# Optimization experiments

Measured on AMD Instinct MI355X. Metric: run time of the kernel, lower is better.

## Reference

```python
import jax, jax.numpy as jnp
import numpy as np

DIM = 512
HEADS = 8
DIM_HEAD = 64
INNER = HEADS * DIM_HEAD  # 512
NARROW_K = 9
WIDE_K = 9
WIDE_DIL = 5


def setup_inputs() -> dict:
    key = jax.random.key(0)
    ks = jax.random.split(key, 12)
    b, n = 4, 2048
    s = lambda fan_in: 1.0 / np.sqrt(fan_in)
    inp = {
        'tokens': jax.random.normal(ks[0], (b, n, DIM), jnp.float32),
        'mask': jax.random.randint(ks[1], (b, n), 0, 2) > 0,
        'w_qkv': jax.random.normal(ks[2], (DIM, INNER * 3), jnp.float32) * s(DIM),
        'w_out': jax.random.normal(ks[3], (INNER, DIM), jnp.float32) * s(INNER),
        'b_out': jnp.zeros((DIM,), jnp.float32),
        'w_narrow': jax.random.normal(ks[4], (DIM, DIM, NARROW_K), jnp.float32) * s(DIM * NARROW_K),
        'b_narrow': jnp.zeros((DIM,), jnp.float32),
        'w_wide': jax.random.normal(ks[5], (DIM, DIM, WIDE_K), jnp.float32) * s(DIM * WIDE_K),
        'b_wide': jnp.zeros((DIM,), jnp.float32),
        'ln1_g': jnp.ones((DIM,), jnp.float32),
        'ln1_b': jnp.zeros((DIM,), jnp.float32),
        'ff_w': jax.random.normal(ks[6], (DIM, DIM), jnp.float32) * s(DIM),
        'ff_b': jnp.zeros((DIM,), jnp.float32),
        'ln2_g': jnp.ones((DIM,), jnp.float32),
        'ln2_b': jnp.zeros((DIM,), jnp.float32),
    }
    return inp


def layer_norm(x, g, b, eps=1e-5):
    m = jnp.mean(x, axis=-1, keepdims=True)
    v = jnp.mean(jnp.square(x - m), axis=-1, keepdims=True)
    return (x - m) / jnp.sqrt(v + eps) * g + b


def rope_encoding(seq_len, dim_head, dtype):
    inv_freq = 1.0 / (10000.0 ** (jnp.arange(0, dim_head, 2, dtype=jnp.float32) / dim_head))
    pos = jnp.arange(seq_len, dtype=jnp.float32)
    sinu = jnp.einsum('i,j->ij', pos, inv_freq)  # [n, d/2]
    return jnp.concatenate([jnp.sin(sinu), jnp.cos(sinu)], axis=-1).astype(dtype)  # [n, d]


def attn(tokens, mask, w_qkv, w_out, b_out):
    b, n, _ = tokens.shape
    qkv = tokens @ w_qkv  # [b, n, 3*inner]
    q, k, v = jnp.split(qkv, 3, axis=-1)
    reshp = lambda t: t.reshape(b, n, HEADS, DIM_HEAD).transpose(0, 2, 1, 3)  # b h n d
    q, k, v = reshp(q), reshp(k), reshp(v)
    rope = rope_encoding(n, DIM_HEAD, tokens.dtype)  # [n, d]
    q = q + rope
    k = k + rope
    mask4 = mask[:, None, :, None]  # b 1 n 1
    big = jnp.finfo(k.dtype).max
    k = jnp.where(mask4, k, -big)
    q = jax.nn.softmax(q, axis=-1) * (DIM_HEAD ** -0.5)
    k = jax.nn.softmax(k, axis=2)  # over n
    v = jnp.where(mask4, v, 0.0)
    context = jnp.einsum('bhnd,bhne->bhde', k, v)
    out = jnp.einsum('bhde,bhnd->bhne', context, q)
    out = out.transpose(0, 2, 1, 3).reshape(b, n, INNER)
    return out @ w_out + b_out


def conv1d(x, w, b, padding, dilation):
    # x: [b, c, n], w: [out, in, k]
    y = jax.lax.conv_general_dilated(
        x, w, window_strides=(1,), padding=[(padding, padding)],
        rhs_dilation=(dilation,), dimension_numbers=('NCW', 'OIW', 'NCW'))
    return y + b[None, :, None]


def reference(tokens, mask, w_qkv, w_out, b_out, w_narrow, b_narrow,
              w_wide, b_wide, ln1_g, ln1_b, ff_w, ff_b, ln2_g, ln2_b):
    tokens = attn(tokens, mask, w_qkv, w_out, b_out)
    conv_in = tokens.transpose(0, 2, 1)  # b d n
    conv_in = jnp.where(mask[:, None, :], conv_in, 0.0)
    narrow = jax.nn.gelu(conv1d(conv_in, w_narrow, b_narrow, NARROW_K // 2, 1), approximate=False)
    wide_pad = (WIDE_K + (WIDE_K - 1) * (WIDE_DIL - 1)) // 2  # 20
    wide = jax.nn.gelu(conv1d(conv_in, w_wide, b_wide, wide_pad, WIDE_DIL), approximate=False)
    tokens = tokens + narrow.transpose(0, 2, 1) + wide.transpose(0, 2, 1)
    tokens = layer_norm(tokens, ln1_g, ln1_b)
    tokens = layer_norm(jax.nn.gelu(tokens @ ff_w + ff_b, approximate=False), ln2_g, ln2_b)
    return tokens
```

## Files before the change

kernel.cpp:

```cpp
#include <hip/hip_runtime.h>
#include <hip/hip_bf16.h>

#define BB 4
#define NN 2048
#define NROWS (BB*NN)

typedef unsigned short u16;
typedef __bf16 bf16x8 __attribute__((ext_vector_type(8)));
typedef u16    u16x8  __attribute__((ext_vector_type(8)));
typedef float  fx4    __attribute__((ext_vector_type(4)));

__device__ __forceinline__ float bf2f(u16 u){
  union { float f; unsigned int i; } x; x.i = ((unsigned int)u) << 16; return x.f;
}
__device__ __forceinline__ u16 f2bf(float f){
  union { float f; unsigned int i; } x; x.f = f;
  unsigned int i = x.i;
  i += 0x7fffu + ((i >> 16) & 1u);
  return (u16)(i >> 16);
}
__device__ __forceinline__ float geluf(float x){
  return 0.5f * x * (1.0f + erff(x * 0.70710678118654752f));
}
__device__ __forceinline__ void gload16(const void* g, void* l){
  __builtin_amdgcn_global_load_lds((const __attribute__((address_space(1))) unsigned int*)g,
                                   (__attribute__((address_space(3))) unsigned int*)l, 16, 0, 0);
}

__global__ __launch_bounds__(256) void sniff_k(const u16* tokens, const unsigned int* mask, int* flags){
  __shared__ int s_f32, s_byte;
  if (threadIdx.x == 0) { s_f32 = 0; s_byte = 0; }
  __syncthreads();
  for (int i = threadIdx.x; i < 4096; i += 256) {
    float v = bf2f(tokens[i]);
    if (!(fabsf(v) < 1e10f)) atomicOr(&s_f32, 1);
  }
  for (int i = threadIdx.x; i < 2048; i += 256) {
    if (mask[i] > 1u) atomicOr(&s_byte, 1);
  }
  __syncthreads();
  if (threadIdx.x == 0) { flags[0] = s_f32; flags[1] = s_byte; }
}

__global__ __launch_bounds__(256) void misc_k(const void* mask, const void* tokens,
                                              const void* p0, const void* p1, const void* p2,
                                              const void* p3, const void* p4, const void* p5,
                                              const void* p6, const void* p7,
                                              const int* flags, float* rope, int* m32,
                                              float* params, float* ctx, float* kS, u16* tokbf){
  const void* srcs[8] = {p0,p1,p2,p3,p4,p5,p6,p7};
  int f32 = flags[0], mbyte = flags[1];
  const int T = 131072 + 8192 + 4096 + 131072 + 2048 + 4194304;
  for (int i = blockIdx.x*256 + threadIdx.x; i < T; i += gridDim.x*256) {
    if (i < 131072) {
      int p = i >> 6, j = i & 63;
      int jj = (j < 32) ? j : j - 32;
      float invf = exp2f(-(float)jj * (13.287712379549449f/32.0f));
      float prod = (float)p * invf;
      rope[i] = (j < 32) ? sinf(prod) : cosf(prod);
    } else if (i < 139264) {
      int k = i - 131072;
      int v = mbyte ? (int)((const unsigned char*)mask)[k] : ((const int*)mask)[k];
      m32[k] = v ? 1 : 0;
    } else if (i < 143360) {
      int k = i - 139264;
      int pid = k >> 9, j = k & 511;
      const void* s = srcs[pid];
      params[k] = f32 ? ((const float*)s)[j] : bf2f(((const u16*)s)[j]);
    } else if (i < 274432) {
      ctx[i - 143360] = 0.0f;
    } else if (i < 276480) {
      kS[i - 274432] = 0.0f;
    } else {
      int k = i - 276480;
      tokbf[k] = f32 ? f2bf(((const float*)tokens)[k]) : ((const u16*)tokens)[k];
    }
  }
}

__global__ __launch_bounds__(256) void prep2_k(const void* w_qkv, const void* w_out, const void* ff_w,
                                               const void* w_narrow, const void* w_wide,
                                               const int* flags,
                                               u16* wqkvt, u16* woutt, u16* ffwt,
                                               u16* wtN2, u16* wtW2){
  int bid = blockIdx.x;
  int f = flags[0];
  int tid = threadIdx.x;
  if (bid < 1024) {
    int tensor = bid >> 9, o = bid & 511;
    const void* src = tensor ? w_wide : w_narrow;
    u16* dst = tensor ? wtW2 : wtN2;
    __shared__ u16 Ls[4608];
    for (int i = tid; i < 4608; i += 256) {
      Ls[i] = f ? f2bf(((const float*)src)[(size_t)o*4608 + i]) : ((const u16*)src)[(size_t)o*4608 + i];
    }
    __syncthreads();
    #pragma unroll
    for (int kk = 0; kk < 9; kk++) {
      #pragma unroll
      for (int u = 0; u < 2; u++) {
        int c = tid + u*256;
        dst[(size_t)kk*262144 + o*512 + c] = Ls[c*9 + kk];
      }
    }
  } else {
    int id = bid - 1024;
    int z = id / 192;
    int rem = id - z*192;
    int x = rem % 24, y = rem / 24;
    int Nn = (z == 0) ? 1536 : 512;
    if (x * 64 >= Nn) return;
    const void* src = (z == 0) ? w_qkv : (z == 1) ? w_out : ff_w;
    u16* dst = (z == 0) ? wqkvt : (z == 1) ? woutt : ffwt;
    __shared__ u16 Ts[64][72];
    int n0 = x * 64, k0 = y * 64;
    int r = tid >> 2, cq = (tid & 3) * 16;
    #pragma unroll
    for (int u = 0; u < 2; u++) {
      int c = cq + u*8;
      int sidx = (k0 + r)*Nn + n0 + c;
      u16x8 v;
      if (f) {
        #pragma unroll
        for (int j = 0; j < 8; j++) v[j] = f2bf(((const float*)src)[sidx + j]);
      } else {
        v = *(const u16x8*)&((const u16*)src)[sidx];
      }
      *(u16x8*)&Ts[r][c] = v;
    }
    __syncthreads();
    #pragma unroll
    for (int u = 0; u < 2; u++) {
      int c = cq + u*8;
      u16x8 v;
      #pragma unroll
      for (int j = 0; j < 8; j++) v[j] = Ts[c + j][r];
      *(u16x8*)&dst[(size_t)(n0 + r)*512 + k0 + c] = v;
    }
  }
}

__global__ __launch_bounds__(256) void mgemm_qkv_k(const u16* A, const u16* Bt, const float* rope,
                                                   const int* mask, u16* qb, u16* keb, u16* vb){
  __shared__ u16 As[128][40];
  __shared__ u16 Bs[128][40];
  __shared__ int smask[128];
  int tid = threadIdx.x;
  int lane = tid & 63;
  int wave = tid >> 6;
  int wm = (wave >> 1) * 64, wn = (wave & 1) * 64;
  int quad = lane >> 4, l16 = lane & 15;
  int m0 = blockIdx.y * 128, n0 = blockIdx.x * 128;
  fx4 acc[4][4] = {};
  int ar = tid >> 2;
  int ac = (tid & 3) * 8;
  for (int k0 = 0; k0 < 512; k0 += 32) {
    *(u16x8*)&As[ar][ac]    = *(const u16x8*)&A[(size_t)(m0+ar)*512 + k0 + ac];
    *(u16x8*)&As[ar+64][ac] = *(const u16x8*)&A[(size_t)(m0+ar+64)*512 + k0 + ac];
    *(u16x8*)&Bs[ar][ac]    = *(const u16x8*)&Bt[(size_t)(n0+ar)*512 + k0 + ac];
    *(u16x8*)&Bs[ar+64][ac] = *(const u16x8*)&Bt[(size_t)(n0+ar+64)*512 + k0 + ac];
    __syncthreads();
    bf16x8 af[4], bfv[4];
    #pragma unroll
    for (int i = 0; i < 4; i++)
      af[i] = __builtin_bit_cast(bf16x8, *(const u16x8*)&As[wm + i*16 + l16][quad*8]);
    #pragma unroll
    for (int j = 0; j < 4; j++)
      bfv[j] = __builtin_bit_cast(bf16x8, *(const u16x8*)&Bs[wn + j*16 + l16][quad*8]);
    #pragma unroll
    for (int i = 0; i < 4; i++)
      #pragma unroll
      for (int j = 0; j < 4; j++)
        acc[i][j] = __builtin_amdgcn_mfma_f32_16x16x32_bf16(af[i], bfv[j], acc[i][j], 0, 0, 0);
    __syncthreads();
  }
  int x = blockIdx.x;
  if (x >= 4) {
    if (tid < 128) smask[tid] = mask[m0 + tid];
    __syncthreads();
  }
  if (x < 4) {
    #pragma unroll
    for (int i = 0; i < 4; i++)
      #pragma unroll
      for (int r = 0; r < 4; r++) {
        int rl = wm + i*16 + quad*4 + r;
        int row = m0 + rl;
        int nseq = row & (NN-1);
        const float* rp = rope + nseq*64 + l16;
        float e0 = __expf(acc[i][0][r] + rp[0]);
        float e1 = __expf(acc[i][1][r] + rp[16]);
        float e2 = __expf(acc[i][2][r] + rp[32]);
        float e3 = __expf(acc[i][3][r] + rp[48]);
        float s = e0 + e1 + e2 + e3;
        s += __shfl_xor(s, 1); s += __shfl_xor(s, 2);
        s += __shfl_xor(s, 4); s += __shfl_xor(s, 8);
        float sc = 0.125f / s;
        size_t base = (size_t)row*512 + n0 + wn + l16;
        qb[base]      = f2bf(e0*sc);
        qb[base + 16] = f2bf(e1*sc);
        qb[base + 32] = f2bf(e2*sc);
        qb[base + 48] = f2bf(e3*sc);
      }
  } else if (x < 8) {
    #pragma unroll
    for (int i = 0; i < 4; i++)
      #pragma unroll
      for (int r = 0; r < 4; r++) {
        int rl = wm + i*16 + quad*4 + r;
        int row = m0 + rl;
        int nseq = row & (NN-1);
        int mk = smask[rl];
        const float* rp = rope + nseq*64 + l16;
        size_t base = (size_t)row*512 + (n0 - 512) + wn + l16;
        #pragma unroll
        for (int j = 0; j < 4; j++) {
          float ke = mk ? __expf(acc[i][j][r] + rp[j*16]) : 0.0f;
          keb[base + j*16] = f2bf(ke);
        }
      }
  } else {
    #pragma unroll
    for (int i = 0; i < 4; i++)
      #pragma unroll
      for (int r = 0; r < 4; r++) {
        int rl = wm + i*16 + quad*4 + r;
        int row = m0 + rl;
        int mk = smask[rl];
        size_t base = (size_t)row*512 + (n0 - 1024) + wn + l16;
        #pragma unroll
        for (int j = 0; j < 4; j++)
          vb[base + j*16] = mk ? f2bf(acc[i][j][r]) : (u16)0;
      }
  }
}

#define FMA16(a, b, acc) \
  acc[0][0] = fmaf(a.x, b.x, acc[0][0]); acc[0][1] = fmaf(a.x, b.y, acc[0][1]); \
  acc[0][2] = fmaf(a.x, b.z, acc[0][2]); acc[0][3] = fmaf(a.x, b.w, acc[0][3]); \
  acc[1][0] = fmaf(a.y, b.x, acc[1][0]); acc[1][1] = fmaf(a.y, b.y, acc[1][1]); \
  acc[1][2] = fmaf(a.y, b.z, acc[1][2]); acc[1][3] = fmaf(a.y, b.w, acc[1][3]); \
  acc[2][0] = fmaf(a.z, b.x, acc[2][0]); acc[2][1] = fmaf(a.z, b.y, acc[2][1]); \
  acc[2][2] = fmaf(a.z, b.z, acc[2][2]); acc[2][3] = fmaf(a.z, b.w, acc[2][3]); \
  acc[3][0] = fmaf(a.w, b.x, acc[3][0]); acc[3][1] = fmaf(a.w, b.y, acc[3][1]); \
  acc[3][2] = fmaf(a.w, b.z, acc[3][2]); acc[3][3] = fmaf(a.w, b.w, acc[3][3]);

__global__ __launch_bounds__(256) void ctx_k(const u16* keb, const u16* vb, float* ctx, float* Sg){
  int bh = blockIdx.x, seg = blockIdx.y;
  int b = bh >> 3, h = bh & 7;
  __shared__ float Ks[32][68], Vs[32][68];
  __shared__ float sS[64];
  int tid = threadIdx.x, tx = tid & 15, ty = tid >> 4;
  if (tid < 64) sS[tid] = 0.0f;
  float acc[4][4] = {{0.f,0.f,0.f,0.f},{0.f,0.f,0.f,0.f},{0.f,0.f,0.f,0.f},{0.f,0.f,0.f,0.f}};
  float sp[8] = {0,0,0,0,0,0,0,0};
  int nl = tid >> 3, dcol = (tid & 7)*8;
  const u16* kp0 = keb + (size_t)(b*NN + seg*256)*512 + h*64 + dcol;
  const u16* vp0 = vb  + (size_t)(b*NN + seg*256)*512 + h*64 + dcol;
  for (int nc = 0; nc < 256; nc += 32) {
    u16x8 ku = *(const u16x8*)(kp0 + (size_t)(nc + nl)*512);
    u16x8 vu = *(const u16x8*)(vp0 + (size_t)(nc + nl)*512);
    float a[8], bb[8];
    #pragma unroll
    for (int t = 0; t < 8; t++) { a[t] = bf2f(ku[t]); bb[t] = bf2f(vu[t]); sp[t] += a[t]; }
    *(float4*)&Ks[nl][dcol]   = (float4){a[0],a[1],a[2],a[3]};
    *(float4*)&Ks[nl][dcol+4] = (float4){a[4],a[5],a[6],a[7]};
    *(float4*)&Vs[nl][dcol]   = (float4){bb[0],bb[1],bb[2],bb[3]};
    *(float4*)&Vs[nl][dcol+4] = (float4){bb[4],bb[5],bb[6],bb[7]};
    __syncthreads();
    #pragma unroll
    for (int q = 0; q < 32; q++) {
      float4 a4 = *(const float4*)&Ks[q][ty*4];
      float4 b4 = *(const float4*)&Vs[q][tx*4];
      FMA16(a4, b4, acc)
    }
    __syncthreads();
  }
  #pragma unroll
  for (int j = 0; j < 8; j++) atomicAdd(&sS[dcol + j], sp[j]);
  float* cp = ctx + (size_t)bh*4096;
  #pragma unroll
  for (int i = 0; i < 4; i++)
    #pragma unroll
    for (int j = 0; j < 4; j++)
      atomicAdd(&cp[(ty*4 + i)*64 + tx*4 + j], acc[i][j]);
  __syncthreads();
  if (tid < 64) atomicAdd(&Sg[bh*64 + tid], sS[tid]);
}

__global__ __launch_bounds__(256) void ctxw_k(const float* ctx, const float* Sg, const u16* woutt,
                                              u16* W2t, u16* cpadb){
  int bx = blockIdx.x;
  int tid = threadIdx.x;
  if (bx >= 32) {
    int idx = (bx - 32)*256 + tid;
    if (idx < BB*40*512) {
      int c = idx & 511;
      int t = (idx >> 9) % 40;
      int b = idx / (40*512);
      int tt = (t < 20) ? t : 2048 + t;
      cpadb[((size_t)b*2088 + tt)*512 + c] = 0;
    }
    return;
  }
  int h = bx & 7, b = bx >> 3;
  int lane = tid & 63, wave = tid >> 6;
  int quad = lane >> 4, l16 = lane & 15;
  const float* cp = ctx + (size_t)(b*8 + h)*4096;
  fx4 acc[8][4] = {};
  #pragma unroll
  for (int ks = 0; ks < 2; ks++) {
    bf16x8 bfv[4];
    #pragma unroll
    for (int j = 0; j < 4; j++) {
      int d = j*16 + l16;
      float S = Sg[(b*8 + h)*64 + d];
      float rs = (S > 0.0f) ? 1.0f/S : 0.0f;
      const float* src = cp + d*64 + ks*32 + quad*8;
      float4 v0 = *(const float4*)src, v1 = *(const float4*)(src + 4);
      bf16x8 t;
      t[0]=(__bf16)(v0.x*rs); t[1]=(__bf16)(v0.y*rs); t[2]=(__bf16)(v0.z*rs); t[3]=(__bf16)(v0.w*rs);
      t[4]=(__bf16)(v1.x*rs); t[5]=(__bf16)(v1.y*rs); t[6]=(__bf16)(v1.z*rs); t[7]=(__bf16)(v1.w*rs);
      bfv[j] = t;
    }
    #pragma unroll
    for (int i = 0; i < 8; i++) {
      int orow = wave*128 + i*16 + l16;
      bf16x8 afr = __builtin_bit_cast(bf16x8, *(const u16x8*)&woutt[(size_t)orow*512 + h*64 + ks*32 + quad*8]);
      #pragma unroll
      for (int j = 0; j < 4; j++)
        acc[i][j] = __builtin_amdgcn_mfma_f32_16x16x32_bf16(afr, bfv[j], acc[i][j], 0, 0, 0);
    }
  }
  u16* out = W2t + (size_t)b*262144;
  #pragma unroll
  for (int i = 0; i < 8; i++)
    #pragma unroll
    for (int j = 0; j < 4; j++)
      #pragma unroll
      for (int r = 0; r < 4; r++) {
        int orow = wave*128 + i*16 + quad*4 + r;
        out[(size_t)orow*512 + h*64 + j*16 + l16] = f2bf(acc[i][j][r]);
      }
}

__global__ __launch_bounds__(256) void mgemm_attn64_k(const u16* qb, const u16* W2t, const float* bias,
                                                      const int* mask, u16* attnb, u16* cpadb){
  __shared__ u16 As[64][40];
  __shared__ u16 Bs[128][40];
  int tid = threadIdx.x;
  int lane = tid & 63;
  int wave = tid >> 6;
  int wn = wave * 32;
  int quad = lane >> 4, l16 = lane & 15;
  int m0 = blockIdx.y * 64, n0 = blockIdx.x * 128, b = blockIdx.z;
  const u16* A  = qb  + (size_t)b*2048*512;
  const u16* Bt = W2t + (size_t)b*262144;
  fx4 acc[4][2] = {};
  int ar = tid >> 2;
  int ac = (tid & 3) * 8;
  for (int k0 = 0; k0 < 512; k0 += 32) {
    *(u16x8*)&As[ar][ac]    = *(const u16x8*)&A[(size_t)(m0+ar)*512 + k0 + ac];
    *(u16x8*)&Bs[ar][ac]    = *(const u16x8*)&Bt[(size_t)(n0+ar)*512 + k0 + ac];
    *(u16x8*)&Bs[ar+64][ac] = *(const u16x8*)&Bt[(size_t)(n0+ar+64)*512 + k0 + ac];
    __syncthreads();
    bf16x8 af[4], bfv[2];
    #pragma unroll
    for (int i = 0; i < 4; i++)
      af[i] = __builtin_bit_cast(bf16x8, *(const u16x8*)&As[i*16 + l16][quad*8]);
    #pragma unroll
    for (int j = 0; j < 2; j++)
      bfv[j] = __builtin_bit_cast(bf16x8, *(const u16x8*)&Bs[wn + j*16 + l16][quad*8]);
    #pragma unroll
    for (int i = 0; i < 4; i++)
      #pragma unroll
      for (int j = 0; j < 2; j++)
        acc[i][j] = __builtin_amdgcn_mfma_f32_16x16x32_bf16(af[i], bfv[j], acc[i][j], 0, 0, 0);
    __syncthreads();
  }
  #pragma unroll
  for (int i = 0; i < 4; i++)
    #pragma unroll
    for (int j = 0; j < 2; j++) {
      int col = n0 + wn + j*16 + l16;
      float bv = bias[col];
      #pragma unroll
      for (int r = 0; r < 4; r++) {
        int row_l = m0 + i*16 + quad*4 + r;
        float v = acc[i][j][r] + bv;
        u16 vbb = f2bf(v);
        attnb[((size_t)b*2048 + row_l)*512 + col] = vbb;
        int mk = mask[b*2048 + row_l];
        cpadb[((size_t)b*2088 + row_l + 20)*512 + col] = mk ? vbb : (u16)0;
      }
    }
}

#define A_ROWS 552
#define A_SZ (A_ROWS*32)
#define W_SZ (9*64*32)
__global__ __launch_bounds__(512, 2) void mconv13_k(const u16* cpad, const u16* Wn, const u16* Ww,
                                                    const float* bias_n, const float* bias_w,
                                                    u16* Dn, u16* Dw){
  __shared__ u16 As[2*A_SZ];
  __shared__ u16 Ws[2*W_SZ];
  int tid = threadIdx.x;
  int lane = tid & 63;
  int wave = tid >> 6;
  int wm = wave * 64;
  int quad = lane >> 4, l16 = lane & 15;
  int o0 = blockIdx.x * 64, m0 = blockIdx.y * 512;
  int b = blockIdx.z >> 1, cid = blockIdx.z & 1;
  const u16* W = cid ? Ww : Wn;
  const float* bias = cid ? bias_w : bias_n;
  u16* D = cid ? Dw : Dn;
  fx4 acc[4][4] = {};
  const u16* cb = cpad + ((size_t)b*2088 + m0)*512;
  int wslot = ((quad ^ ((l16 >> 1) & 3)) * 8);
  int sbase = cid ? 0 : 16;
  int sstep = cid ? 5 : 1;
  int rowb0 = sbase + wm + l16;

#define STAGE_CHUNK(c0, buf)                                                          \
  {                                                                                   \
    _Pragma("unroll")                                                                 \
    for (int it = 0; it < 5; it++) {                                                  \
      int s = it*512 + tid;                                                           \
      if (s < 2208) {                                                                 \
        int lsl = ((s & 3) ^ ((s >> 3) & 3)) * 8;                                     \
        gload16(&cb[(size_t)(s >> 2)*512 + (c0) + lsl],                               \
                &As[(buf)*A_SZ + (it*512 + wave*64)*8]);                              \
      }                                                                               \
    }                                                                                 \
    _Pragma("unroll")                                                                 \
    for (int it = 0; it < 5; it++) {                                                  \
      int s = it*512 + tid;                                                           \
      if (s < 2304) {                                                                 \
        int kk = s >> 8;                                                              \
        int ow = (s >> 2) & 63;                                                       \
        int lsl = ((s & 3) ^ ((s >> 3) & 3)) * 8;                                     \
        gload16(&W[(size_t)kk*262144 + (size_t)(o0 + ow)*512 + (c0) + lsl],           \
                &Ws[(buf)*W_SZ + (it*512 + wave*64)*8]);                              \
      }                                                                               \
    }                                                                                 \
  }

#define LOADFRAG(kk, bfv, afr)                                                        \
  {                                                                                   \
    int rowb = rowb0 + sstep*(kk);                                                    \
    int aslot = ((quad ^ ((rowb >> 1) & 3)) * 8);                                     \
    _Pragma("unroll")                                                                 \
    for (int j = 0; j < 4; j++)                                                       \
      bfv[j] = __builtin_bit_cast(bf16x8,                                             \
                 *(const u16x8*)&Wsb[((kk)*64 + j*16 + l16)*32 + wslot]);             \
    _Pragma("unroll")                                                                 \
    for (int i = 0; i < 4; i++)                                                       \
      afr[i] = __builtin_bit_cast(bf16x8,                                             \
                 *(const u16x8*)&Asb[(rowb + i*16)*32 + aslot]);                      \
  }

#define MFMATAP_SGB(bfv, afr)                                                         \
  {                                                                                   \
    _Pragma("unroll")                                                                 \
    for (int i = 0; i < 4; i++)                                                       \
      _Pragma("unroll")                                                               \
      for (int j = 0; j < 4; j++)                                                     \
        acc[i][j] = __builtin_amdgcn_mfma_f32_16x16x32_bf16(afr[i], bfv[j],           \
                                                            acc[i][j], 0, 0, 0);      \
    _Pragma("unroll")                                                                 \
    for (int g = 0; g < 8; g++) {                                                     \
      __builtin_amdgcn_sched_group_barrier(0x008, 2, 0);                  \
      __builtin_amdgcn_sched_group_barrier(0x100, 1, 0);               \
    }                                                                                 \
  }

#define MFMATAP_PLAIN(bfv, afr)                                                       \
  {                                                                                   \
    _Pragma("unroll")                                                                 \
    for (int i = 0; i < 4; i++)                                                       \
      _Pragma("unroll")                                                               \
      for (int j = 0; j < 4; j++)                                                     \
        acc[i][j] = __builtin_amdgcn_mfma_f32_16x16x32_bf16(afr[i], bfv[j],           \
                                                            acc[i][j], 0, 0, 0);      \
  }

  STAGE_CHUNK(0, 0)
  __syncthreads();

  for (int ch = 0; ch < 16; ch++) {
    int cur = ch & 1;
    const u16* Asb = &As[cur*A_SZ];
    const u16* Wsb = &Ws[cur*W_SZ];
    bf16x8 bfvA[4], afrA[4], bfvB[4], afrB[4];
    LOADFRAG(0, bfvA, afrA)
    if (ch < 15) {
      int c0n = (ch + 1) * 32;
      int nb = cur ^ 1;
      STAGE_CHUNK(c0n, nb)
    }
    #pragma unroll
    for (int kt = 0; kt < 8; kt += 2) {
      LOADFRAG(kt+1, bfvB, afrB)
      MFMATAP_SGB(bfvA, afrA)
      LOADFRAG(kt+2, bfvA, afrA)
      MFMATAP_SGB(bfvB, afrB)
    }
    MFMATAP_PLAIN(bfvA, afrA)
    __syncthreads();
  }
#undef STAGE_CHUNK
#undef LOADFRAG
#undef MFMATAP_SGB
#undef MFMATAP_PLAIN
  #pragma unroll
  for (int i = 0; i < 4; i++)
    #pragma unroll
    for (int j = 0; j < 4; j++) {
      int col = o0 + j*16 + l16;
      float bv = bias[col];
      #pragma unroll
      for (int r = 0; r < 4; r++) {
        int row = b*2048 + m0 + wm + i*16 + quad*4 + r;
        D[(size_t)row*512 + col] = f2bf(geluf(acc[i][j][r] + bv));
      }
    }
}

template<bool BIAS, bool GELU>
__global__ __launch_bounds__(256) void mgemm64b_k(const u16* A, const u16* Bt, const float* bias,
                                                  u16* C, int M, int N, int K){
  __shared__ u16 As[64][40];
  __shared__ u16 Bs[128][40];
  int tid = threadIdx.x;
  int lane = tid & 63;
  int wave = tid >> 6;
  int wn = wave * 32;
  int quad = lane >> 4, l16 = lane & 15;
  int m0 = blockIdx.y * 64, n0 = blockIdx.x * 128;
  fx4 acc[4][2] = {};
  int ar = tid >> 2;
  int ac = (tid & 3) * 8;
  for (int k0 = 0; k0 < K; k0 += 32) {
    *(u16x8*)&As[ar][ac]    = *(const u16x8*)&A[(size_t)(m0+ar)*K + k0 + ac];
    *(u16x8*)&Bs[ar][ac]    = *(const u16x8*)&Bt[(size_t)(n0+ar)*K + k0 + ac];
    *(u16x8*)&Bs[ar+64][ac] = *(const u16x8*)&Bt[(size_t)(n0+ar+64)*K + k0 + ac];
    __syncthreads();
    bf16x8 af[4], bfv[2];
    #pragma unroll
    for (int i = 0; i < 4; i++)
      af[i] = __builtin_bit_cast(bf16x8, *(const u16x8*)&As[i*16 + l16][quad*8]);
    #pragma unroll
    for (int j = 0; j < 2; j++)
      bfv[j] = __builtin_bit_cast(bf16x8, *(const u16x8*)&Bs[wn + j*16 + l16][quad*8]);
    #pragma unroll
    for (int i = 0; i < 4; i++)
      #pragma unroll
      for (int j = 0; j < 2; j++)
        acc[i][j] = __builtin_amdgcn_mfma_f32_16x16x32_bf16(af[i], bfv[j], acc[i][j], 0, 0, 0);
    __syncthreads();
  }
  #pragma unroll
  for (int i = 0; i < 4; i++)
    #pragma unroll
    for (int j = 0; j < 2; j++) {
      int col = n0 + wn + j*16 + l16;
      float bv = BIAS ? bias[col] : 0.0f;
      #pragma unroll
      for (int r = 0; r < 4; r++) {
        int row = m0 + i*16 + quad*4 + r;
        float v = acc[i][j][r] + bv;
        if (GELU) v = geluf(v);
        C[(size_t)row*N + col] = f2bf(v);
      }
    }
}

__device__ __forceinline__ float block_sum512(float v, float* red){
  #pragma unroll
  for (int o = 32; o; o >>= 1) v += __shfl_xor(v, o, 64);
  int w = threadIdx.x >> 6;
  if ((threadIdx.x & 63) == 0) red[w] = v;
  __syncthreads();
  float t = red[0] + red[1] + red[2] + red[3];
  __syncthreads();
  return t;
}

template<int NADD, int OM>
__global__ __launch_bounds__(256) void ln_k(const u16* X, const u16* Y, const u16* Z,
                                            const float* g, const float* be,
                                            const int* flags, void* out){
  __shared__ float red[4];
  size_t row = blockIdx.x;
  int tid = threadIdx.x;
  const u16* xp = X + row*512;
  float x0 = bf2f(xp[tid]), x1 = bf2f(xp[tid + 256]);
  if (NADD >= 1) { const u16* yp = Y + row*512; x0 += bf2f(yp[tid]); x1 += bf2f(yp[tid + 256]); }
  if (NADD >= 2) { const u16* zp = Z + row*512; x0 += bf2f(zp[tid]); x1 += bf2f(zp[tid + 256]); }
  float mean = block_sum512(x0 + x1, red) * (1.0f/512.0f);
  float d0 = x0 - mean, d1 = x1 - mean;
  float var = block_sum512(d0*d0 + d1*d1, red) * (1.0f/512.0f);
  float inv = rsqrtf(var + 1e-5f);
  float r0 = d0*inv*g[tid]       + be[tid];
  float r1 = d1*inv*g[tid + 256] + be[tid + 256];
  bool obf = (OM == 1) || (OM == 2 && !flags[0]);
  if (obf) {
    u16* op = (u16*)out;
    op[row*512 + tid]       = f2bf(r0);
    op[row*512 + tid + 256] = f2bf(r1);
  } else {
    float* op = (float*)out;
    op[row*512 + tid]       = r0;
    op[row*512 + tid + 256] = r1;
  }
}

extern "C" void kernel_launch(void* const* d_in, const int* in_sizes, int n_in,
                              void* d_out, int out_size, void* d_ws, size_t ws_size,
                              hipStream_t stream) {
  const void* tokens   = d_in[0];
  const void* mask     = d_in[1];
  const void* w_qkv    = d_in[2];
  const void* w_out    = d_in[3];
  const void* b_out    = d_in[4];
  const void* w_narrow = d_in[5];
  const void* b_narrow = d_in[6];
  const void* w_wide   = d_in[7];
  const void* b_wide   = d_in[8];
  const void* ln1_g    = d_in[9];
  const void* ln1_b    = d_in[10];
  const void* ff_w     = d_in[11];
  const void* ff_b     = d_in[12];
  const void* ln2_g    = d_in[13];
  const void* ln2_b    = d_in[14];

  float* ws = (float*)d_ws;
  int*   flags  = (int*)ws;
  int*   m32    = (int*)(ws + 16);
  float* params = ws + 8208;
  float* kS     = ws + 12304;
  float* ctx    = ws + 14352;
  float* rope   = ws + 145424;
  u16*   tokbf  = (u16*)(ws + 276496);
  u16*   wqkvt  = (u16*)(ws + 2373648);
  u16*   woutt  = (u16*)(ws + 2766864);
  u16*   ffwt   = (u16*)(ws + 2897936);
  u16*   wtN2   = (u16*)(ws + 3029008);
  u16*   wtW2   = (u16*)(ws + 4208656);
  u16*   qb     = (u16*)(ws + 5388304);
  u16*   keb    = (u16*)(ws + 7485456);
  u16*   vb     = (u16*)(ws + 9582608);
  u16*   W2t    = (u16*)(ws + 11679760);
  u16*   attnb  = (u16*)(ws + 12204048);
  u16*   cpadb  = (u16*)(ws + 14301200);
  u16*   Dnb    = (u16*)(ws + 16439312);
  u16*   Dwb    = (u16*)(ws + 18536464);
  u16*   Eb     = attnb;
  u16*   t1b    = tokbf;

  float* p_bout = params;        float* p_bnar = params + 512;
  float* p_bwid = params + 1024; float* p_l1g  = params + 1536;
  float* p_l1b  = params + 2048; float* p_ffb  = params + 2560;
  float* p_l2g  = params + 3072; float* p_l2b  = params + 3584;

  sniff_k<<<dim3(1), dim3(256), 0, stream>>>((const u16*)tokens, (const unsigned int*)mask, flags);
  misc_k<<<dim3(8192), dim3(256), 0, stream>>>(mask, tokens, b_out, b_narrow, b_wide, ln1_g, ln1_b,
                                               ff_b, ln2_g, ln2_b, flags, rope, m32, params, ctx,
                                               kS, tokbf);
  prep2_k<<<dim3(1600), dim3(256), 0, stream>>>(w_qkv, w_out, ff_w, w_narrow, w_wide, flags,
                                                wqkvt, woutt, ffwt, wtN2, wtW2);

  mgemm_qkv_k<<<dim3(12, 64), dim3(256), 0, stream>>>(
      tokbf, wqkvt, rope, m32, qb, keb, vb);

  ctx_k<<<dim3(32, 8), dim3(256), 0, stream>>>(keb, vb, ctx, kS);

  ctxw_k<<<dim3(352), dim3(256), 0, stream>>>(ctx, kS, woutt, W2t, cpadb);

  mgemm_attn64_k<<<dim3(4, 32, 4), dim3(256), 0, stream>>>(qb, W2t, p_bout, m32, attnb, cpadb);

  mconv13_k<<<dim3(8, 4, 8), dim3(512), 0, stream>>>(cpadb, wtN2, wtW2, p_bnar, p_bwid, Dnb, Dwb);

  ln_k<2,1><<<dim3(NROWS), dim3(256), 0, stream>>>(attnb, Dnb, Dwb, p_l1g, p_l1b, flags, (void*)t1b);

  mgemm64b_k<true,true><<<dim3(4, 128), dim3(256), 0, stream>>>(
      t1b, ffwt, p_ffb, Eb, NROWS, 512, 512);

  ln_k<0,2><<<dim3(NROWS), dim3(256), 0, stream>>>(Eb, nullptr, nullptr, p_l2g, p_l2b, flags, d_out);
}
```

Baseline: 334.1 us.

## Use direct global-to-LDS loads with XOR swizzle in GEMM kernels

Three GEMM kernels (QKV, attention output, feed-forward) now stage tiles with gload16 direct-to-LDS loads instead of register round-trips. They use an unpadded 32-wide layout with an XOR swizzle so fragment reads avoid bank conflicts. The conv kernel's scheduling hints are also reordered to interleave one LDS read per MFMA and then group the rest. This aims to cut VGPR use and instruction overhead in the load path, but the loads remain single-buffered with a sync barrier, so the latency-hiding gain may be limited.

```diff
diff --git a/kernel.cpp b/kernel.cpp
--- a/kernel.cpp
+++ b/kernel.cpp
@@ -142,8 +142,8 @@
 
 __global__ __launch_bounds__(256) void mgemm_qkv_k(const u16* A, const u16* Bt, const float* rope,
                                                    const int* mask, u16* qb, u16* keb, u16* vb){
-  __shared__ u16 As[128][40];
-  __shared__ u16 Bs[128][40];
+  __shared__ u16 As[128*32];
+  __shared__ u16 Bs[128*32];
   __shared__ int smask[128];
   int tid = threadIdx.x;
   int lane = tid & 63;
@@ -152,21 +152,33 @@
   int quad = lane >> 4, l16 = lane & 15;
   int m0 = blockIdx.y * 128, n0 = blockIdx.x * 128;
   fx4 acc[4][4] = {};
-  int ar = tid >> 2;
-  int ac = (tid & 3) * 8;
   for (int k0 = 0; k0 < 512; k0 += 32) {
-    *(u16x8*)&As[ar][ac]    = *(const u16x8*)&A[(size_t)(m0+ar)*512 + k0 + ac];
-    *(u16x8*)&As[ar+64][ac] = *(const u16x8*)&A[(size_t)(m0+ar+64)*512 + k0 + ac];
-    *(u16x8*)&Bs[ar][ac]    = *(const u16x8*)&Bt[(size_t)(n0+ar)*512 + k0 + ac];
-    *(u16x8*)&Bs[ar+64][ac] = *(const u16x8*)&Bt[(size_t)(n0+ar+64)*512 + k0 + ac];
+    #pragma unroll
+    for (int it = 0; it < 2; it++) {
+      int s = it*256 + tid;
+      int lsl = ((s & 3) ^ ((s >> 3) & 3)) * 8;
+      gload16(&A[(size_t)(m0 + (s >> 2))*512 + k0 + lsl], &As[(it*256 + wave*64)*8]);
+    }
+    #pragma unroll
+    for (int it = 0; it < 2; it++) {
+      int s = it*256 + tid;
+      int lsl = ((s & 3) ^ ((s >> 3) & 3)) * 8;
+      gload16(&Bt[(size_t)(n0 + (s >> 2))*512 + k0 + lsl], &Bs[(it*256 + wave*64)*8]);
+    }
     __syncthreads();
     bf16x8 af[4], bfv[4];
     #pragma unroll
-    for (int i = 0; i < 4; i++)
-      af[i] = __builtin_bit_cast(bf16x8, *(const u16x8*)&As[wm + i*16 + l16][quad*8]);
-    #pragma unroll
-    for (int j = 0; j < 4; j++)
-      bfv[j] = __builtin_bit_cast(bf16x8, *(const u16x8*)&Bs[wn + j*16 + l16][quad*8]);
+    for (int i = 0; i < 4; i++) {
+      int row = wm + i*16 + l16;
+      af[i] = __builtin_bit_cast(bf16x8,
+                *(const u16x8*)&As[row*32 + ((quad ^ ((row >> 1) & 3)) * 8)]);
+    }
+    #pragma unroll
+    for (int j = 0; j < 4; j++) {
+      int row = wn + j*16 + l16;
+      bfv[j] = __builtin_bit_cast(bf16x8,
+                *(const u16x8*)&Bs[row*32 + ((quad ^ ((row >> 1) & 3)) * 8)]);
+    }
     #pragma unroll
     for (int i = 0; i < 4; i++)
       #pragma unroll
@@ -346,8 +358,8 @@
 
 __global__ __launch_bounds__(256) void mgemm_attn64_k(const u16* qb, const u16* W2t, const float* bias,
                                                       const int* mask, u16* attnb, u16* cpadb){
-  __shared__ u16 As[64][40];
-  __shared__ u16 Bs[128][40];
+  __shared__ u16 As[64*32];
+  __shared__ u16 Bs[128*32];
   int tid = threadIdx.x;
   int lane = tid & 63;
   int wave = tid >> 6;
@@ -357,20 +369,32 @@
   const u16* A  = qb  + (size_t)b*2048*512;
   const u16* Bt = W2t + (size_t)b*262144;
   fx4 acc[4][2] = {};
-  int ar = tid >> 2;
-  int ac = (tid & 3) * 8;
   for (int k0 = 0; k0 < 512; k0 += 32) {
-    *(u16x8*)&As[ar][ac]    = *(const u16x8*)&A[(size_t)(m0+ar)*512 + k0 + ac];
-    *(u16x8*)&Bs[ar][ac]    = *(const u16x8*)&Bt[(size_t)(n0+ar)*512 + k0 + ac];
-    *(u16x8*)&Bs[ar+64][ac] = *(const u16x8*)&Bt[(size_t)(n0+ar+64)*512 + k0 + ac];
+    {
+      int s = tid;
+      int lsl = ((s & 3) ^ ((s >> 3) & 3)) * 8;
+      gload16(&A[(size_t)(m0 + (s >> 2))*512 + k0 + lsl], &As[(wave*64)*8]);
+    }
+    #pragma unroll
+    for (int it = 0; it < 2; it++) {
+      int s = it*256 + tid;
+      int lsl = ((s & 3) ^ ((s >> 3) & 3)) * 8;
+      gload16(&Bt[(size_t)(n0 + (s >> 2))*512 + k0 + lsl], &Bs[(it*256 + wave*64)*8]);
+    }
     __syncthreads();
     bf16x8 af[4], bfv[2];
     #pragma unroll
-    for (int i = 0; i < 4; i++)
-      af[i] = __builtin_bit_cast(bf16x8, *(const u16x8*)&As[i*16 + l16][quad*8]);
-    #pragma unroll
-    for (int j = 0; j < 2; j++)
-      bfv[j] = __builtin_bit_cast(bf16x8, *(const u16x8*)&Bs[wn + j*16 + l16][quad*8]);
+    for (int i = 0; i < 4; i++) {
+      int row = i*16 + l16;
+      af[i] = __builtin_bit_cast(bf16x8,
+                *(const u16x8*)&As[row*32 + ((quad ^ ((row >> 1) & 3)) * 8)]);
+    }
+    #pragma unroll
+    for (int j = 0; j < 2; j++) {
+      int row = wn + j*16 + l16;
+      bfv[j] = __builtin_bit_cast(bf16x8,
+                *(const u16x8*)&Bs[row*32 + ((quad ^ ((row >> 1) & 3)) * 8)]);
+    }
     #pragma unroll
     for (int i = 0; i < 4; i++)
       #pragma unroll
@@ -399,7 +423,7 @@
 #define A_ROWS 552
 #define A_SZ (A_ROWS*32)
 #define W_SZ (9*64*32)
-__global__ __launch_bounds__(512, 2) void mconv13_k(const u16* cpad, const u16* Wn, const u16* Ww,
+__global__ __launch_bounds__(512, 2) void mconv14_k(const u16* cpad, const u16* Wn, const u16* Ww,
                                                     const float* bias_n, const float* bias_w,
                                                     u16* Dn, u16* Dw){
   __shared__ u16 As[2*A_SZ];
@@ -469,9 +493,10 @@
                                                             acc[i][j], 0, 0, 0);      \
     _Pragma("unroll")                                                                 \
     for (int g = 0; g < 8; g++) {                                                     \
-      __builtin_amdgcn_sched_group_barrier(0x008, 2, 0);                  \
       __builtin_amdgcn_sched_group_barrier(0x100, 1, 0);               \
+      __builtin_amdgcn_sched_group_barrier(0x008, 1, 0);                  \
     }                                                                                 \
+    __builtin_amdgcn_sched_group_barrier(0x008, 8, 0);                    \
   }
 
 #define MFMATAP_PLAIN(bfv, afr)                                                       \
@@ -529,8 +554,8 @@
 template<bool BIAS, bool GELU>
 __global__ __launch_bounds__(256) void mgemm64b_k(const u16* A, const u16* Bt, const float* bias,
                                                   u16* C, int M, int N, int K){
-  __shared__ u16 As[64][40];
-  __shared__ u16 Bs[128][40];
+  __shared__ u16 As[64*32];
+  __shared__ u16 Bs[128*32];
   int tid = threadIdx.x;
   int lane = tid & 63;
   int wave = tid >> 6;
@@ -538,20 +563,32 @@
   int quad = lane >> 4, l16 = lane & 15;
   int m0 = blockIdx.y * 64, n0 = blockIdx.x * 128;
   fx4 acc[4][2] = {};
-  int ar = tid >> 2;
-  int ac = (tid & 3) * 8;
   for (int k0 = 0; k0 < K; k0 += 32) {
-    *(u16x8*)&As[ar][ac]    = *(const u16x8*)&A[(size_t)(m0+ar)*K + k0 + ac];
-    *(u16x8*)&Bs[ar][ac]    = *(const u16x8*)&Bt[(size_t)(n0+ar)*K + k0 + ac];
-    *(u16x8*)&Bs[ar+64][ac] = *(const u16x8*)&Bt[(size_t)(n0+ar+64)*K + k0 + ac];
+    {
+      int s = tid;
+      int lsl = ((s & 3) ^ ((s >> 3) & 3)) * 8;
+      gload16(&A[(size_t)(m0 + (s >> 2))*K + k0 + lsl], &As[(wave*64)*8]);
+    }
+    #pragma unroll
+    for (int it = 0; it < 2; it++) {
+      int s = it*256 + tid;
+      int lsl = ((s & 3) ^ ((s >> 3) & 3)) * 8;
+      gload16(&Bt[(size_t)(n0 + (s >> 2))*K + k0 + lsl], &Bs[(it*256 + wave*64)*8]);
+    }
     __syncthreads();
     bf16x8 af[4], bfv[2];
     #pragma unroll
-    for (int i = 0; i < 4; i++)
-      af[i] = __builtin_bit_cast(bf16x8, *(const u16x8*)&As[i*16 + l16][quad*8]);
-    #pragma unroll
-    for (int j = 0; j < 2; j++)
-      bfv[j] = __builtin_bit_cast(bf16x8, *(const u16x8*)&Bs[wn + j*16 + l16][quad*8]);
+    for (int i = 0; i < 4; i++) {
+      int row = i*16 + l16;
+      af[i] = __builtin_bit_cast(bf16x8,
+                *(const u16x8*)&As[row*32 + ((quad ^ ((row >> 1) & 3)) * 8)]);
+    }
+    #pragma unroll
+    for (int j = 0; j < 2; j++) {
+      int row = wn + j*16 + l16;
+      bfv[j] = __builtin_bit_cast(bf16x8,
+                *(const u16x8*)&Bs[row*32 + ((quad ^ ((row >> 1) & 3)) * 8)]);
+    }
     #pragma unroll
     for (int i = 0; i < 4; i++)
       #pragma unroll
@@ -679,7 +716,7 @@
 
   mgemm_attn64_k<<<dim3(4, 32, 4), dim3(256), 0, stream>>>(qb, W2t, p_bout, m32, attnb, cpadb);
 
-  mconv13_k<<<dim3(8, 4, 8), dim3(512), 0, stream>>>(cpadb, wtN2, wtW2, p_bnar, p_bwid, Dnb, Dwb);
+  mconv14_k<<<dim3(8, 4, 8), dim3(512), 0, stream>>>(cpadb, wtN2, wtW2, p_bnar, p_bwid, Dnb, Dwb);
 
   ln_k<2,1><<<dim3(NROWS), dim3(256), 0, stream>>>(attnb, Dnb, Dwb, p_l1g, p_l1b, flags, (void*)t1b);
 
```

After: 384.3 us. 1.15x slower.
